# Kernel optimization log

Measured on AMD Instinct MI355X. Metric: run time of the kernel, lower is better.

The kernel has to match this reference:

```python
import jax, jax.numpy as jnp
import numpy as np

N, E, F_IN, E_IN, HID, H, C, L, OUT = 20000, 320000, 128, 64, 64, 4, 64, 4, 32


def setup_inputs() -> dict:
    key = jax.random.key(0)
    ks = jax.random.split(key, 24)
    s = 0.05
    return {
        'x': jax.random.normal(ks[0], (N, F_IN), jnp.float32),
        'edge_index': jax.random.randint(ks[1], (2, E), 0, N, jnp.int32),
        'edge_attr': jax.random.normal(ks[2], (E, E_IN), jnp.float32),
        'node_W': jax.random.normal(ks[3], (F_IN, HID), jnp.float32) * s,
        'node_b': jnp.zeros((HID,), jnp.float32),
        'eenc_W': jax.random.normal(ks[4], (E_IN, HID), jnp.float32) * s,
        'eenc_b': jnp.zeros((HID,), jnp.float32),
        'Wq': jax.random.normal(ks[5], (L, HID, H * C), jnp.float32) * s,
        'bq': jnp.zeros((L, H * C), jnp.float32),
        'Wk': jax.random.normal(ks[6], (L, HID, H * C), jnp.float32) * s,
        'bk': jnp.zeros((L, H * C), jnp.float32),
        'Wv': jax.random.normal(ks[7], (L, HID, H * C), jnp.float32) * s,
        'bv': jnp.zeros((L, H * C), jnp.float32),
        'We': jax.random.normal(ks[8], (L, HID, H * C), jnp.float32) * s,  # lin_edge, bias=False in PyG
        'Wskip': jax.random.normal(ks[9], (L, HID, HID), jnp.float32) * s,
        'bskip': jnp.zeros((L, HID), jnp.float32),
        'ln_g': jnp.ones((L, HID), jnp.float32),
        'ln_b': jnp.zeros((L, HID), jnp.float32),
        'lin_W': jax.random.normal(ks[10], (HID, OUT), jnp.float32) * s,
        'lin_b': jnp.zeros((OUT,), jnp.float32),
    }


def _layernorm(h, g, b):
    mu = h.mean(-1, keepdims=True)
    var = ((h - mu) ** 2).mean(-1, keepdims=True)
    return (h - mu) * jax.lax.rsqrt(var + 1e-5) * g + b


def _transformer_conv(h, ea, src, dst, Wq, bq, Wk, bk, Wv, bv, We, Wskip, bskip):
    n = h.shape[0]
    q = (h @ Wq + bq).reshape(n, H, C)[dst]          # [E,H,C] dst (x_i)
    k = (h @ Wk + bk).reshape(n, H, C)[src]          # [E,H,C] src (x_j)
    v = (h @ Wv + bv).reshape(n, H, C)[src]
    e = (ea @ We).reshape(-1, H, C)                  # per-edge features
    k = k + e
    alpha = (q * k).sum(-1) * (1.0 / jnp.sqrt(jnp.float32(C)))   # [E,H]
    amax = jax.ops.segment_max(alpha, dst, num_segments=n)       # segment softmax over dst
    ex = jnp.exp(alpha - amax[dst])
    denom = jax.ops.segment_sum(ex, dst, num_segments=n)
    a = ex / (denom[dst] + 1e-16)
    msg = (v + e) * a[..., None]                     # [E,H,C]
    out = jax.ops.segment_sum(msg, dst, num_segments=n)          # [N,H,C]
    out = out.mean(axis=1)                           # concat=False -> head mean
    return out + (h @ Wskip + bskip)                 # root_weight skip


def reference(x, edge_index, edge_attr, node_W, node_b, eenc_W, eenc_b,
              Wq, bq, Wk, bk, Wv, bv, We, Wskip, bskip, ln_g, ln_b, lin_W, lin_b):
    src, dst = edge_index[0], edge_index[1]
    h = x @ node_W + node_b
    ea = edge_attr @ eenc_W + eenc_b
    # layer 0: conv only (per the forward body)
    h = _transformer_conv(h, ea, src, dst, Wq[0], bq[0], Wk[0], bk[0], Wv[0], bv[0],
                          We[0], Wskip[0], bskip[0])
    # layers 1..L-1: res+ block (norm -> relu -> [dropout=id at eval] -> conv -> +res)
    for l in range(1, L):
        res = h
        z = _layernorm(h, ln_g[l], ln_b[l])
        z = jax.nn.relu(z)
        z = _transformer_conv(z, ea, src, dst, Wq[l], bq[l], Wk[l], bk[l], Wv[l], bv[l],
                              We[l], Wskip[l], bskip[l])
        h = z + res
    h = _layernorm(h, ln_g[0], ln_b[0])
    h = jax.nn.relu(h)
    return h @ lin_W + lin_b
```

## Files before the change

kernel.cpp:

```cpp
#include <hip/hip_runtime.h>
#include <hip/hip_fp16.h>
#include <math.h>

#define N_NODES 20000
#define N_EDGES 320000
#define F_IN    128
#define E_IN    64
#define HID     64
#define NH      4
#define CH      64
#define HC      256
#define L_LAYERS 4
#define OUT_DIM 32
#define WCOLS   1088

typedef _Float16 half8 __attribute__((ext_vector_type(8)));
typedef float f32x4 __attribute__((ext_vector_type(4)));

__global__ __launch_bounds__(256) void hist_dst(const int* __restrict__ dst,
                                                int* __restrict__ hist) {
    int e = blockIdx.x * 256 + threadIdx.x;
    if (e < N_EDGES) atomicAdd(&hist[dst[e]], 1);
}

__global__ __launch_bounds__(1024) void build_order(const int* __restrict__ hist,
                                                    int* __restrict__ node_order,
                                                    int* __restrict__ rank_of,
                                                    int* __restrict__ deg_rank,
                                                    int* __restrict__ new_rp,
                                                    int* __restrict__ cursor2) {
    __shared__ int bins[256];
    __shared__ int curb[256];
    __shared__ int sums[1024];
    int t = threadIdx.x;
    if (t < 256) bins[t] = 0;
    __syncthreads();
    for (int n = t; n < N_NODES; n += 1024) {
        int d = hist[n]; if (d > 255) d = 255;
        atomicAdd(&bins[d], 1);
    }
    __syncthreads();
    if (t < 256) {
        int acc = 0;
        for (int b = t + 1; b < 256; b++) acc += bins[b];
        curb[t] = acc;
    }
    __syncthreads();
    for (int n = t; n < N_NODES; n += 1024) {
        int d = hist[n];
        int b = d > 255 ? 255 : d;
        int r = atomicAdd(&curb[b], 1);
        node_order[r] = n;
        rank_of[n] = r;
        deg_rank[r] = d;
    }
    __syncthreads();
    const int CHUNK = 20;
    int base = t * CHUNK;
    int local[CHUNK];
    int s = 0;
    for (int i = 0; i < CHUNK; i++) {
        int idx = base + i;
        int vv = (idx < N_NODES) ? deg_rank[idx] : 0;
        local[i] = s;
        s += vv;
    }
    sums[t] = s;
    __syncthreads();
    for (int off = 1; off < 1024; off <<= 1) {
        int v = (t >= off) ? sums[t - off] : 0;
        __syncthreads();
        sums[t] += v;
        __syncthreads();
    }
    int excl = (t == 0) ? 0 : sums[t - 1];
    for (int i = 0; i < CHUNK; i++) {
        int idx = base + i;
        if (idx < N_NODES) {
            int p = excl + local[i];
            new_rp[idx] = p;
            cursor2[idx] = p;
        }
    }
    if (t == 1023) new_rp[N_NODES] = sums[1023];
}

__global__ __launch_bounds__(256) void compute_pos(const int* __restrict__ src,
                                                   const int* __restrict__ dst,
                                                   const int* __restrict__ rank_of,
                                                   int* __restrict__ cursor2,
                                                   int* __restrict__ eid_of,
                                                   int* __restrict__ srcrank_perm) {
    int e = blockIdx.x * 256 + threadIdx.x;
    if (e >= N_EDGES) return;
    int r = rank_of[dst[e]];
    int pos = atomicAdd(&cursor2[r], 1);
    eid_of[pos] = e;
    srcrank_perm[pos] = rank_of[src[e]];
}

__global__ __launch_bounds__(256) void permute_attr(const int* __restrict__ eid_of,
                                                    const float* __restrict__ eattr,
                                                    __half* __restrict__ attr_p) {
    int t = threadIdx.x;
    int wave = t >> 6, lane = t & 63;
    int p = blockIdx.x * 16 + wave * 4 + (lane >> 4);
    if (p >= N_EDGES) return;
    int e = eid_of[p];
    int qi = (lane & 15) * 4;
    float4 a = *(const float4*)(eattr + (size_t)e * E_IN + qi);
    __half2 h0 = __floats2half2_rn(a.x, a.y);
    __half2 h1 = __floats2half2_rn(a.z, a.w);
    uint2 packed;
    packed.x = *(unsigned int*)&h0;
    packed.y = *(unsigned int*)&h1;
    *(uint2*)(attr_p + (size_t)p * E_IN + qi) = packed;
}

__global__ __launch_bounds__(256) void make_wqeA(const float* __restrict__ Wq,
                                                 const float* __restrict__ bq,
                                                 const float* __restrict__ We,
                                                 const float* __restrict__ eW,
                                                 const float* __restrict__ eb,
                                                 float* __restrict__ Wqe2,
                                                 float* __restrict__ bqe2,
                                                 float* __restrict__ wqb,
                                                 float* __restrict__ bqb) {
    int l = blockIdx.x / HID, i = blockIdx.x % HID;
    int t = threadIdx.x;
    int h = t >> 6, j = t & 63;
    __shared__ float wrow[256];
    __shared__ float brow[256];
    const float* WqL = Wq + (size_t)l * HID * HC;
    const float* WeL = We + (size_t)l * HID * HC;
    float acc = 0.f;
    for (int c = 0; c < CH; c++)
        acc += WqL[i * HC + h * CH + c] * WeL[j * HC + h * CH + c];
    wrow[t] = acc;
    if (i == 0) {
        const float* bqL = bq + l * HC;
        float ab = 0.f;
        for (int c = 0; c < CH; c++)
            ab += bqL[h * CH + c] * WeL[j * HC + h * CH + c];
        brow[t] = ab;
    }
    __syncthreads();
    int h2 = t >> 6, m = t & 63;
    float a2 = 0.f;
    for (int jj = 0; jj < HID; jj++) a2 += wrow[h2 * 64 + jj] * eW[m * HID + jj];
    Wqe2[(size_t)l * HID * HC + i * HC + t] = a2;
    if (m == 0) {
        float aw = 0.f;
        for (int jj = 0; jj < HID; jj++) aw += wrow[h2 * 64 + jj] * eb[jj];
        wqb[l * HID * NH + i * NH + h2] = aw;
    }
    if (i == 0) {
        float ab2 = 0.f;
        for (int jj = 0; jj < HID; jj++) ab2 += brow[h2 * 64 + jj] * eW[m * HID + jj];
        bqe2[l * HC + t] = ab2;
        if (m == 0) {
            float bb = 0.f;
            for (int jj = 0; jj < HID; jj++) bb += brow[h2 * 64 + jj] * eb[jj];
            bqb[l * NH + h2] = bb;
        }
    }
}

__global__ __launch_bounds__(256) void make_weE16(const float* __restrict__ eW,
                                                  const float* __restrict__ eb,
                                                  const float* __restrict__ We,
                                                  _Float16* __restrict__ WeE16T,
                                                  float* __restrict__ beE) {
    int l = blockIdx.x / E_IN, m = blockIdx.x % E_IN;
    int t = threadIdx.x;
    const float* WeL = We + (size_t)l * HID * HC;
    float acc = 0.f;
    for (int j = 0; j < HID; j++) acc += eW[m * HID + j] * WeL[j * HC + t];
    WeE16T[((size_t)l * HC + t) * 64 + m] = (_Float16)acc;
    if (m == 0) {
        float a = 0.f;
        for (int j = 0; j < HID; j++) a += eb[j] * WeL[j * HC + t];
        beE[l * HC + t] = a;
    }
}

__global__ __launch_bounds__(256) void make_w16(
        const float* __restrict__ Wq, const float* __restrict__ Wk,
        const float* __restrict__ Wv, const float* __restrict__ Wqe2,
        const float* __restrict__ Wsk,
        const float* __restrict__ bq, const float* __restrict__ bk,
        const float* __restrict__ bv, const float* __restrict__ bqe2,
        const float* __restrict__ bsk,
        _Float16* __restrict__ W16T, float* __restrict__ biasc) {
    int l = blockIdx.x / 272;
    int cg = blockIdx.x % 272;
    int col = cg * 4 + (threadIdx.x >> 6);
    int i = threadIdx.x & 63;
    float w, b;
    if (col < 512) {
        int c = (col >> 3) * 4 + (col & 3);
        if ((col >> 2) & 1) { w = Wqe2[(size_t)l*HID*HC + i*HC + c]; b = bqe2[l*HC + c]; }
        else                { w = Wq[(size_t)l*HID*HC + i*HC + c];   b = bq[l*HC + c]; }
    } else if (col < 1024) {
        int cc = col - 512;
        int c = (cc >> 3) * 4 + (cc & 3);
        if ((cc >> 2) & 1) { w = Wv[(size_t)l*HID*HC + i*HC + c]; b = bv[l*HC + c]; }
        else               { w = Wk[(size_t)l*HID*HC + i*HC + c]; b = bk[l*HC + c]; }
    } else {
        int c = col - 1024;
        w = Wsk[(size_t)l*HID*HID + i*HID + c];  b = bsk[l*HID + c];
    }
    W16T[((size_t)l * WCOLS + col) * 64 + i] = (_Float16)w;
    if (i == 0) biasc[l * WCOLS + col] = b;
}

__global__ __launch_bounds__(256) void make_w0(const float* __restrict__ nW,
                                               const float* __restrict__ nb,
                                               _Float16* __restrict__ W0T,
                                               float* __restrict__ b0) {
    int col = blockIdx.x * 2 + (threadIdx.x >> 7);
    int i = threadIdx.x & 127;
    W0T[col * F_IN + i] = (_Float16)nW[i * HID + col];
    if (i == 0) b0[col] = nb[col];
}

__global__ __launch_bounds__(256) void node_pre0(const float* __restrict__ x,
        const int* __restrict__ node_order,
        const _Float16* __restrict__ W0T, const float* __restrict__ b0,
        const _Float16* __restrict__ W16T, const float* __restrict__ biasc,
        const float* __restrict__ wqb, const float* __restrict__ bqb,
        _Float16* __restrict__ qqw, _Float16* __restrict__ kv,
        float* __restrict__ skip, float* __restrict__ qb) {
    int t = threadIdx.x;
    int wave = t >> 6, lane = t & 63;
    int quad = lane >> 4, mrow = lane & 15;
    int base = blockIdx.x * 32;
    __shared__ _Float16 xs[32][136];
    __shared__ _Float16 zs[32][72];
    __shared__ int nord[32];
    if (t < 32) nord[t] = node_order[base + t];
    __syncthreads();
    for (int it = 0; it < 4; it++) {
        int idx = it * 256 + t;
        int m = idx >> 5, c4 = idx & 31;
        float4 a = *(const float4*)(x + (size_t)nord[m] * F_IN + c4 * 4);
        _Float16* d = &xs[m][c4 * 4];
        d[0] = (_Float16)a.x; d[1] = (_Float16)a.y;
        d[2] = (_Float16)a.z; d[3] = (_Float16)a.w;
    }
    __syncthreads();
    {
        int col = wave * 16 + mrow;
        const _Float16* w0row = W0T + (size_t)col * F_IN;
        f32x4 acc0 = {0.f, 0.f, 0.f, 0.f};
        f32x4 acc1 = {0.f, 0.f, 0.f, 0.f};
#pragma unroll
        for (int kk = 0; kk < 4; kk++) {
            half8 bfrag = *(const half8*)(w0row + kk * 32 + quad * 8);
            half8 af0 = *(const half8*)&xs[mrow][kk * 32 + quad * 8];
            half8 af1 = *(const half8*)&xs[16 + mrow][kk * 32 + quad * 8];
            acc0 = __builtin_amdgcn_mfma_f32_16x16x32_f16(af0, bfrag, acc0, 0, 0, 0);
            acc1 = __builtin_amdgcn_mfma_f32_16x16x32_f16(af1, bfrag, acc1, 0, 0, 0);
        }
        float bb = b0[col];
#pragma unroll
        for (int reg = 0; reg < 4; reg++) {
            zs[quad * 4 + reg][col] = (_Float16)(acc0[reg] + bb);
            zs[16 + quad * 4 + reg][col] = (_Float16)(acc1[reg] + bb);
        }
    }
    __syncthreads();
    if (t < 128) {
        int m = t >> 2, h4 = t & 3;
        float a = bqb[h4];
        for (int i = 0; i < HID; i++) a += (float)zs[m][i] * wqb[i * NH + h4];
        qb[(base + m) * NH + h4] = a;
    }
    half8 a00 = *(const half8*)&zs[mrow][quad * 8];
    half8 a01 = *(const half8*)&zs[mrow][32 + quad * 8];
    half8 a10 = *(const half8*)&zs[16 + mrow][quad * 8];
    half8 a11 = *(const half8*)&zs[16 + mrow][32 + quad * 8];
    int colwave = wave * 272;
    for (int tile = 0; tile < 17; tile++) {
        int colb = colwave + tile * 16;
        int col = colb + mrow;
        const _Float16* wrow = W16T + (size_t)col * 64;
        half8 b0f = *(const half8*)(wrow + quad * 8);
        half8 b1f = *(const half8*)(wrow + 32 + quad * 8);
        f32x4 acc0 = {0.f, 0.f, 0.f, 0.f};
        f32x4 acc1 = {0.f, 0.f, 0.f, 0.f};
        acc0 = __builtin_amdgcn_mfma_f32_16x16x32_f16(a00, b0f, acc0, 0, 0, 0);
        acc0 = __builtin_amdgcn_mfma_f32_16x16x32_f16(a01, b1f, acc0, 0, 0, 0);
        acc1 = __builtin_amdgcn_mfma_f32_16x16x32_f16(a10, b0f, acc1, 0, 0, 0);
        acc1 = __builtin_amdgcn_mfma_f32_16x16x32_f16(a11, b1f, acc1, 0, 0, 0);
        float bi = biasc[col];
        int seg = colb >> 9;
        int r0 = base + quad * 4;
#pragma unroll
        for (int reg = 0; reg < 4; reg++) {
            float v0 = acc0[reg] + bi;
            float v1 = acc1[reg] + bi;
            int ra = r0 + reg, rb = ra + 16;
            if (colb >= 1024) {
                int c = col - 1024;
                skip[ra * HID + c] = v0;
                skip[rb * HID + c] = v1;
            } else if (seg == 0) {
                qqw[(size_t)ra * 512 + col] = (_Float16)v0;
                qqw[(size_t)rb * 512 + col] = (_Float16)v1;
            } else {
                int c = col - 512;
                kv[(size_t)ra * 512 + c] = (_Float16)v0;
                kv[(size_t)rb * 512 + c] = (_Float16)v1;
            }
        }
    }
}

__global__ __launch_bounds__(256) void gather_edges(
        const int* __restrict__ new_rp,
        const int* __restrict__ srcrank_perm, const __half* __restrict__ attr_p,
        const __half* __restrict__ kv,
        const float* __restrict__ qb,
        const __half* qqw,
        float* numv, __half* __restrict__ numea16,
        float* __restrict__ den) {
    int wave = threadIdx.x >> 6;
    int lane = threadIdx.x & 63;
    int r = blockIdx.x * 4 + wave;
    if (r >= N_NODES) return;
    int e0 = new_rp[r], e1 = new_rp[r + 1];
    int qi = (lane & 15) * 4;
    int head = lane >> 4;
    uint4 qr = *(const uint4*)(qqw + (size_t)r * 512 + lane * 8);
    float2 q01 = __half22float2(*(__half2*)&qr.x);
    float2 q23 = __half22float2(*(__half2*)&qr.y);
    float2 w01 = __half22float2(*(__half2*)&qr.z);
    float2 w23 = __half22float2(*(__half2*)&qr.w);
    float qbh = qb[r * NH + head];
    float4 nv = make_float4(0.f, 0.f, 0.f, 0.f);
    float4 ne = make_float4(0.f, 0.f, 0.f, 0.f);
    float dsum = 0.f;
#pragma unroll 2
    for (int e = e0; e < e1; e++) {
        int s_ = srcrank_perm[e];
        uint2 araw = *(const uint2*)(attr_p + (size_t)e * E_IN + qi);
        uint4 kraw = *(const uint4*)(kv + (size_t)s_ * (2 * HC) + lane * 8);
        float2 a01 = __half22float2(*(__half2*)&araw.x);
        float2 a23 = __half22float2(*(__half2*)&araw.y);
        float2 k01 = __half22float2(*(__half2*)&kraw.x);
        float2 k23 = __half22float2(*(__half2*)&kraw.y);
        float2 v01 = __half22float2(*(__half2*)&kraw.z);
        float2 v23 = __half22float2(*(__half2*)&kraw.w);
        float rr = q01.x * k01.x + q01.y * k01.y + q23.x * k23.x + q23.y * k23.y
                 + w01.x * a01.x + w01.y * a01.y + w23.x * a23.x + w23.y * a23.y;
        rr += __shfl_xor(rr, 1);
        rr += __shfl_xor(rr, 2);
        rr += __shfl_xor(rr, 4);
        rr += __shfl_xor(rr, 8);
        float ex = __expf((rr + qbh) * 0.125f);
        nv.x += ex * v01.x; nv.y += ex * v01.y; nv.z += ex * v23.x; nv.w += ex * v23.y;
        ne.x += ex * a01.x; ne.y += ex * a01.y; ne.z += ex * a23.x; ne.w += ex * a23.y;
        dsum += ex;
    }
    *(float4*)(numv + (size_t)r * HC + lane * 4) = nv;
    __half2 n01 = __floats2half2_rn(ne.x, ne.y);
    __half2 n23 = __floats2half2_rn(ne.z, ne.w);
    uint2 np;
    np.x = *(unsigned int*)&n01;
    np.y = *(unsigned int*)&n23;
    *(uint2*)(numea16 + (size_t)r * HC + lane * 4) = np;
    if ((lane & 15) == 0) den[r * NH + head] = dsum;
}

__global__ __launch_bounds__(256) void node_mid(
        const int* __restrict__ node_order,
        const float* numv,
        const __half* __restrict__ numea16,
        const float* __restrict__ den_g,
        float* skip,
        float* __restrict__ h,
        const _Float16* __restrict__ WeE16T,
        const float* __restrict__ beE,
        int add_res,
        const _Float16* __restrict__ W16T,
        const float* __restrict__ biasc,
        const float* __restrict__ wqb, const float* __restrict__ bqb,
        const float* __restrict__ g, const float* __restrict__ be,
        _Float16* qqw, _Float16* __restrict__ kv,
        float* __restrict__ qb) {
    int t = threadIdx.x;
    int wave = t >> 6, lane = t & 63;
    int quad = lane >> 4, mrow = lane & 15;
    int base = blockIdx.x * 16;
    __shared__ _Float16 ea16[16][264];
    __shared__ float hsum[4][16][64];
    __shared__ float hnew[16][64];
    __shared__ _Float16 zs[16][72];
    __shared__ float bsh[256];
    __shared__ float dsh[64];
    __shared__ int nord[16];
    if (t < 16) nord[t] = node_order[base + t];
    if (t < 64) dsh[t] = den_g[base * 4 + t];
    bsh[t] = beE[t];
    for (int it = 0; it < 2; it++) {
        int idx = it * 256 + t;
        int m = idx >> 5, c8 = idx & 31;
        uint4 raw = *(const uint4*)(numea16 + (size_t)(base + m) * HC + c8 * 8);
        *(uint4*)&ea16[m][c8 * 8] = raw;
    }
    __syncthreads();
    {
        int hd = wave;
        half8 a_lo = *(const half8*)&ea16[mrow][hd * 64 + quad * 8];
        half8 a_hi = *(const half8*)&ea16[mrow][hd * 64 + 32 + quad * 8];
        for (int nt = 0; nt < 4; nt++) {
            int c = nt * 16 + mrow;
            const _Float16* bp = WeE16T + (size_t)(hd * 64 + c) * 64;
            half8 b_lo = *(const half8*)(bp + quad * 8);
            half8 b_hi = *(const half8*)(bp + 32 + quad * 8);
            f32x4 acc = {0.f, 0.f, 0.f, 0.f};
            acc = __builtin_amdgcn_mfma_f32_16x16x32_f16(a_lo, b_lo, acc, 0, 0, 0);
            acc = __builtin_amdgcn_mfma_f32_16x16x32_f16(a_hi, b_hi, acc, 0, 0, 0);
            int tp = hd * 64 + c;
#pragma unroll
            for (int reg = 0; reg < 4; reg++) {
                int m = quad * 4 + reg;
                float nvv = numv[(size_t)(base + m) * HC + tp];
                float dd = dsh[m * 4 + hd];
                hsum[hd][m][c] = (nvv + acc[reg] + dd * bsh[tp]) / (dd + 1e-16f) * 0.25f;
            }
        }
    }
    __syncthreads();
    for (int it = 0; it < 4; it++) {
        int idx = it * 256 + t;
        int m = idx >> 6, c = idx & 63;
        float s = hsum[0][m][c] + hsum[1][m][c] + hsum[2][m][c] + hsum[3][m][c]
                + skip[(base + m) * HID + c];
        if (add_res) s += h[nord[m] * HID + c];
        h[nord[m] * HID + c] = s;
        hnew[m][c] = s;
    }
    __syncthreads();
    for (int it = 0; it < 4; it++) {
        int m = it * 4 + wave;
        float val = hnew[m][lane];
        float mu = val;
        for (int o = 32; o > 0; o >>= 1) mu += __shfl_xor(mu, o);
        mu *= (1.f / 64.f);
        float d = val - mu;
        float var = d * d;
        for (int o = 32; o > 0; o >>= 1) var += __shfl_xor(var, o);
        var *= (1.f / 64.f);
        val = fmaxf(d * rsqrtf(var + 1e-5f) * g[lane] + be[lane], 0.f);
        zs[m][lane] = (_Float16)val;
    }
    __syncthreads();
    if (t < 64) {
        int m = t >> 2, h4 = t & 3;
        float a = bqb[h4];
        for (int i = 0; i < HID; i++) a += (float)zs[m][i] * wqb[i * NH + h4];
        qb[(base + m) * NH + h4] = a;
    }
    half8 a00 = *(const half8*)&zs[mrow][quad * 8];
    half8 a01 = *(const half8*)&zs[mrow][32 + quad * 8];
    int colwave = wave * 272;
    for (int tile = 0; tile < 17; tile++) {
        int colb = colwave + tile * 16;
        int col = colb + mrow;
        const _Float16* wrow = W16T + (size_t)col * 64;
        half8 b0f = *(const half8*)(wrow + quad * 8);
        half8 b1f = *(const half8*)(wrow + 32 + quad * 8);
        f32x4 acc = {0.f, 0.f, 0.f, 0.f};
        acc = __builtin_amdgcn_mfma_f32_16x16x32_f16(a00, b0f, acc, 0, 0, 0);
        acc = __builtin_amdgcn_mfma_f32_16x16x32_f16(a01, b1f, acc, 0, 0, 0);
        float bi = biasc[col];
        int seg = colb >> 9;
#pragma unroll
        for (int reg = 0; reg < 4; reg++) {
            float v0 = acc[reg] + bi;
            int ra = base + quad * 4 + reg;
            if (colb >= 1024) {
                skip[ra * HID + (col - 1024)] = v0;
            } else if (seg == 0) {
                qqw[(size_t)ra * 512 + col] = (_Float16)v0;
            } else {
                kv[(size_t)ra * 512 + (col - 512)] = (_Float16)v0;
            }
        }
    }
}

__global__ __launch_bounds__(256) void node_fin(
        const int* __restrict__ node_order,
        const float* __restrict__ numv,
        const __half* __restrict__ numea16,
        const float* __restrict__ den_g,
        const float* __restrict__ skip,
        const float* __restrict__ h,
        const _Float16* __restrict__ WeE16T, const float* __restrict__ beE,
        const float* __restrict__ g, const float* __restrict__ be,
        const float* __restrict__ linW, const float* __restrict__ linb,
        float* __restrict__ out) {
    int t = threadIdx.x;
    int wave = t >> 6, lane = t & 63;
    int quad = lane >> 4, mrow = lane & 15;
    int base = blockIdx.x * 16;
    __shared__ _Float16 ea16[16][264];
    __shared__ float hsum[4][16][64];
    __shared__ float hnew[16][64];
    __shared__ float bsh[256];
    __shared__ float dsh[64];
    __shared__ int nord[16];
    if (t < 16) nord[t] = node_order[base + t];
    if (t < 64) dsh[t] = den_g[base * 4 + t];
    bsh[t] = beE[t];
    for (int it = 0; it < 2; it++) {
        int idx = it * 256 + t;
        int m = idx >> 5, c8 = idx & 31;
        uint4 raw = *(const uint4*)(numea16 + (size_t)(base + m) * HC + c8 * 8);
        *(uint4*)&ea16[m][c8 * 8] = raw;
    }
    __syncthreads();
    {
        int hd = wave;
        half8 a_lo = *(const half8*)&ea16[mrow][hd * 64 + quad * 8];
        half8 a_hi = *(const half8*)&ea16[mrow][hd * 64 + 32 + quad * 8];
        for (int nt = 0; nt < 4; nt++) {
            int c = nt * 16 + mrow;
            const _Float16* bp = WeE16T + (size_t)(hd * 64 + c) * 64;
            half8 b_lo = *(const half8*)(bp + quad * 8);
            half8 b_hi = *(const half8*)(bp + 32 + quad * 8);
            f32x4 acc = {0.f, 0.f, 0.f, 0.f};
            acc = __builtin_amdgcn_mfma_f32_16x16x32_f16(a_lo, b_lo, acc, 0, 0, 0);
            acc = __builtin_amdgcn_mfma_f32_16x16x32_f16(a_hi, b_hi, acc, 0, 0, 0);
            int tp = hd * 64 + c;
#pragma unroll
            for (int reg = 0; reg < 4; reg++) {
                int m = quad * 4 + reg;
                float nvv = numv[(size_t)(base + m) * HC + tp];
                float dd = dsh[m * 4 + hd];
                hsum[hd][m][c] = (nvv + acc[reg] + dd * bsh[tp]) / (dd + 1e-16f) * 0.25f;
            }
        }
    }
    __syncthreads();
    for (int it = 0; it < 4; it++) {
        int idx = it * 256 + t;
        int m = idx >> 6, c = idx & 63;
        float s = hsum[0][m][c] + hsum[1][m][c] + hsum[2][m][c] + hsum[3][m][c]
                + skip[(base + m) * HID + c] + h[nord[m] * HID + c];
        hnew[m][c] = s;
    }
    __syncthreads();
    for (int it = 0; it < 4; it++) {
        int m = it * 4 + wave;
        float val = hnew[m][lane];
        float mu = val;
        for (int o = 32; o > 0; o >>= 1) mu += __shfl_xor(mu, o);
        mu *= (1.f / 64.f);
        float d = val - mu;
        float var = d * d;
        for (int o = 32; o > 0; o >>= 1) var += __shfl_xor(var, o);
        var *= (1.f / 64.f);
        hnew[m][lane] = fmaxf(d * rsqrtf(var + 1e-5f) * g[lane] + be[lane], 0.f);
    }
    __syncthreads();
    for (int it = 0; it < 2; it++) {
        int idx = it * 256 + t;
        int m = idx >> 5, col = idx & 31;
        float a = linb[col];
        for (int i = 0; i < HID; i++) a += hnew[m][i] * linW[i * OUT_DIM + col];
        out[nord[m] * OUT_DIM + col] = a;
    }
}

extern "C" void kernel_launch(void* const* d_in, const int* in_sizes, int n_in,
                              void* d_out, int out_size, void* d_ws, size_t ws_size,
                              hipStream_t stream) {
    const float* x      = (const float*)d_in[0];
    const int*   ei     = (const int*)d_in[1];
    const float* eattr  = (const float*)d_in[2];
    const float* node_W = (const float*)d_in[3];
    const float* node_b = (const float*)d_in[4];
    const float* eenc_W = (const float*)d_in[5];
    const float* eenc_b = (const float*)d_in[6];
    const float* Wq     = (const float*)d_in[7];
    const float* bq     = (const float*)d_in[8];
    const float* Wk     = (const float*)d_in[9];
    const float* bk     = (const float*)d_in[10];
    const float* Wv     = (const float*)d_in[11];
    const float* bv     = (const float*)d_in[12];
    const float* We     = (const float*)d_in[13];
    const float* Wskip  = (const float*)d_in[14];
    const float* bskip  = (const float*)d_in[15];
    const float* ln_g   = (const float*)d_in[16];
    const float* ln_b   = (const float*)d_in[17];
    const float* lin_W  = (const float*)d_in[18];
    const float* lin_b  = (const float*)d_in[19];
    float* out = (float*)d_out;

    const int* src = ei;
    const int* dst = ei + N_EDGES;

    float* ws = (float*)d_ws;
    __half* attr_p = (__half*)ws; ws += (size_t)N_EDGES * E_IN / 2;
    float* h    = ws; ws += N_NODES * HID;
    _Float16* qqw = (_Float16*)ws; ws += (size_t)N_NODES * HC;
    float* numv = (float*)qqw;
    __half* numea16 = (__half*)ws; ws += (size_t)N_NODES * HC / 2;
    _Float16* kv = (_Float16*)ws; ws += (size_t)N_NODES * HC;
    float* skip = ws; ws += N_NODES * HID;
    float* den  = ws; ws += N_NODES * NH;
    float* qb   = ws; ws += N_NODES * NH;
    float* Wqe2 = ws; ws += (size_t)L_LAYERS * HID * HC;
    float* bqe2 = ws; ws += L_LAYERS * HC;
    float* wqb  = ws; ws += L_LAYERS * HID * NH;
    float* bqb  = ws; ws += L_LAYERS * NH;
    _Float16* WeE16T = (_Float16*)ws; ws += (size_t)L_LAYERS * HC * HID / 2;
    float* beE  = ws; ws += L_LAYERS * HC;
    _Float16* W16T = (_Float16*)ws; ws += (size_t)L_LAYERS * WCOLS * HID / 2;
    float* biasc = ws; ws += L_LAYERS * WCOLS;
    _Float16* W0T = (_Float16*)ws; ws += HID * F_IN / 2;
    float* b0  = ws; ws += HID;
    int* ip = (int*)ws;
    int* hist         = ip; ip += N_NODES;
    int* node_order   = ip; ip += N_NODES;
    int* rank_of      = ip; ip += N_NODES;
    int* deg_rank     = ip; ip += N_NODES;
    int* new_rp       = ip; ip += N_NODES + 4;
    int* cursor2      = ip; ip += N_NODES;
    int* srcrank_perm = ip; ip += N_EDGES;
    int* eid_of       = ip; ip += N_EDGES;

    hipMemsetAsync(hist, 0, N_NODES * sizeof(int), stream);
    hist_dst<<<(N_EDGES + 255) / 256, 256, 0, stream>>>(dst, hist);
    build_order<<<1, 1024, 0, stream>>>(hist, node_order, rank_of, deg_rank,
                                        new_rp, cursor2);

    make_wqeA<<<L_LAYERS * HID, 256, 0, stream>>>(Wq, bq, We, eenc_W, eenc_b,
                                                  Wqe2, bqe2, wqb, bqb);
    make_weE16<<<L_LAYERS * E_IN, 256, 0, stream>>>(eenc_W, eenc_b, We, WeE16T, beE);
    make_w16<<<L_LAYERS * 272, 256, 0, stream>>>(Wq, Wk, Wv, Wqe2, Wskip,
                                                 bq, bk, bv, bqe2, bskip,
                                                 W16T, biasc);
    make_w0<<<HID / 2, 256, 0, stream>>>(node_W, node_b, W0T, b0);

    compute_pos<<<(N_EDGES + 255) / 256, 256, 0, stream>>>(src, dst, rank_of, cursor2,
                                                           eid_of, srcrank_perm);
    permute_attr<<<N_EDGES / 16, 256, 0, stream>>>(eid_of, eattr, attr_p);

    node_pre0<<<N_NODES / 32, 256, 0, stream>>>(
        x, node_order, W0T, b0, W16T, biasc, wqb, bqb, qqw, kv, skip, qb);

    for (int l = 0; l < L_LAYERS; l++) {
        gather_edges<<<(N_NODES + 3) / 4, 256, 0, stream>>>(
            new_rp, srcrank_perm, attr_p, (const __half*)kv, qb,
            (const __half*)qqw, numv, numea16, den);
        if (l < L_LAYERS - 1) {
            node_mid<<<N_NODES / 16, 256, 0, stream>>>(
                node_order, numv, numea16, den, skip, h,
                WeE16T + (size_t)l * HC * HID, beE + l * HC,
                (l > 0) ? 1 : 0,
                W16T + (size_t)(l + 1) * WCOLS * HID, biasc + (l + 1) * WCOLS,
                wqb + (l + 1) * HID * NH, bqb + (l + 1) * NH,
                ln_g + (l + 1) * HID, ln_b + (l + 1) * HID,
                qqw, kv, qb);
        } else {
            node_fin<<<N_NODES / 16, 256, 0, stream>>>(
                node_order, numv, numea16, den, skip, h,
                WeE16T + (size_t)l * HC * HID, beE + l * HC,
                ln_g, ln_b, lin_W, lin_b, out);
        }
    }
}
```

Baseline: 733.6 us.

## Fold head-mean into edge-weight GEMM and vectorize node projection stores

The per-head edge-feature GEMM plus the 4-way hsum reduction is replaced by one K=256 MFMA against a concatenated weight matrix. The 1/den scaling is applied to the edge aggregates before the GEMM, so the head mean falls out of the matrix product. The projection GEMMs swap MFMA operand order so each lane holds four consecutive columns, which allows half4/float4 stores instead of scalar scattered stores. The q-bias reduction is split across more threads with shuffles, and h is kept in rank order, which drops the node_order indirection in node_mid. In exchange, aggregates are rescaled in fp16 before the matmul, which may shift precision slightly.

```diff
diff --git a/kernel.cpp b/kernel.cpp
--- a/kernel.cpp
+++ b/kernel.cpp
@@ -15,6 +15,7 @@
 #define WCOLS   1088
 
 typedef _Float16 half8 __attribute__((ext_vector_type(8)));
+typedef _Float16 half4 __attribute__((ext_vector_type(4)));
 typedef float f32x4 __attribute__((ext_vector_type(4)));
 
 __global__ __launch_bounds__(256) void hist_dst(const int* __restrict__ dst,
@@ -166,21 +167,27 @@
     }
 }
 
-__global__ __launch_bounds__(256) void make_weE16(const float* __restrict__ eW,
-                                                  const float* __restrict__ eb,
-                                                  const float* __restrict__ We,
-                                                  _Float16* __restrict__ WeE16T,
-                                                  float* __restrict__ beE) {
-    int l = blockIdx.x / E_IN, m = blockIdx.x % E_IN;
+__global__ __launch_bounds__(256) void make_wcat(const float* __restrict__ eW,
+                                                 const float* __restrict__ eb,
+                                                 const float* __restrict__ We,
+                                                 _Float16* __restrict__ Wcat16,
+                                                 float* __restrict__ beE) {
+    int l = blockIdx.x / 64, c = blockIdx.x % 64;
     int t = threadIdx.x;
-    const float* WeL = We + (size_t)l * HID * HC;
+    __shared__ float sh[4][64];
+    {
+        int j = t & 63, h = t >> 6;
+        sh[h][j] = We[(size_t)l * HID * HC + j * HC + h * 64 + c];
+    }
+    __syncthreads();
+    int h = t >> 6, m = t & 63;
     float acc = 0.f;
-    for (int j = 0; j < HID; j++) acc += eW[m * HID + j] * WeL[j * HC + t];
-    WeE16T[((size_t)l * HC + t) * 64 + m] = (_Float16)acc;
-    if (m == 0) {
+    for (int j = 0; j < HID; j++) acc += eW[m * HID + j] * sh[h][j];
+    Wcat16[((size_t)l * 64 + c) * 256 + t] = (_Float16)acc;
+    if (t < 4) {
         float a = 0.f;
-        for (int j = 0; j < HID; j++) a += eb[j] * WeL[j * HC + t];
-        beE[l * HC + t] = a;
+        for (int j = 0; j < HID; j++) a += eb[j] * sh[t][j];
+        beE[l * HC + t * 64 + c] = a;
     }
 }
 
@@ -250,31 +257,35 @@
     }
     __syncthreads();
     {
-        int col = wave * 16 + mrow;
-        const _Float16* w0row = W0T + (size_t)col * F_IN;
+        int colb = wave * 16;
+        const _Float16* w0row = W0T + (size_t)(colb + mrow) * F_IN;
         f32x4 acc0 = {0.f, 0.f, 0.f, 0.f};
         f32x4 acc1 = {0.f, 0.f, 0.f, 0.f};
 #pragma unroll
         for (int kk = 0; kk < 4; kk++) {
-            half8 bfrag = *(const half8*)(w0row + kk * 32 + quad * 8);
-            half8 af0 = *(const half8*)&xs[mrow][kk * 32 + quad * 8];
-            half8 af1 = *(const half8*)&xs[16 + mrow][kk * 32 + quad * 8];
-            acc0 = __builtin_amdgcn_mfma_f32_16x16x32_f16(af0, bfrag, acc0, 0, 0, 0);
-            acc1 = __builtin_amdgcn_mfma_f32_16x16x32_f16(af1, bfrag, acc1, 0, 0, 0);
-        }
-        float bb = b0[col];
-#pragma unroll
-        for (int reg = 0; reg < 4; reg++) {
-            zs[quad * 4 + reg][col] = (_Float16)(acc0[reg] + bb);
-            zs[16 + quad * 4 + reg][col] = (_Float16)(acc1[reg] + bb);
-        }
-    }
-    __syncthreads();
-    if (t < 128) {
-        int m = t >> 2, h4 = t & 3;
-        float a = bqb[h4];
-        for (int i = 0; i < HID; i++) a += (float)zs[m][i] * wqb[i * NH + h4];
-        qb[(base + m) * NH + h4] = a;
+            half8 wfrag = *(const half8*)(w0row + kk * 32 + quad * 8);
+            half8 xf0 = *(const half8*)&xs[mrow][kk * 32 + quad * 8];
+            half8 xf1 = *(const half8*)&xs[16 + mrow][kk * 32 + quad * 8];
+            acc0 = __builtin_amdgcn_mfma_f32_16x16x32_f16(wfrag, xf0, acc0, 0, 0, 0);
+            acc1 = __builtin_amdgcn_mfma_f32_16x16x32_f16(wfrag, xf1, acc1, 0, 0, 0);
+        }
+        float4 bb = *(const float4*)(b0 + colb + quad * 4);
+        half4 h0v = {(_Float16)(acc0[0] + bb.x), (_Float16)(acc0[1] + bb.y),
+                     (_Float16)(acc0[2] + bb.z), (_Float16)(acc0[3] + bb.w)};
+        half4 h1v = {(_Float16)(acc1[0] + bb.x), (_Float16)(acc1[1] + bb.y),
+                     (_Float16)(acc1[2] + bb.z), (_Float16)(acc1[3] + bb.w)};
+        *(half4*)&zs[mrow][colb + quad * 4] = h0v;
+        *(half4*)&zs[16 + mrow][colb + quad * 4] = h1v;
+    }
+    __syncthreads();
+    {
+        int p = t >> 1, s4 = t & 1;
+        int m = p >> 2, h4 = p & 3;
+        float a = 0.f;
+        for (int i = s4 * 32; i < s4 * 32 + 32; i++)
+            a += (float)zs[m][i] * wqb[i * NH + h4];
+        a += __shfl_xor(a, 1);
+        if (s4 == 0) qb[(base + m) * NH + h4] = a + bqb[h4];
     }
     half8 a00 = *(const half8*)&zs[mrow][quad * 8];
     half8 a01 = *(const half8*)&zs[mrow][32 + quad * 8];
@@ -283,35 +294,34 @@
     int colwave = wave * 272;
     for (int tile = 0; tile < 17; tile++) {
         int colb = colwave + tile * 16;
-        int col = colb + mrow;
-        const _Float16* wrow = W16T + (size_t)col * 64;
+        const _Float16* wrow = W16T + (size_t)(colb + mrow) * 64;
         half8 b0f = *(const half8*)(wrow + quad * 8);
         half8 b1f = *(const half8*)(wrow + 32 + quad * 8);
         f32x4 acc0 = {0.f, 0.f, 0.f, 0.f};
         f32x4 acc1 = {0.f, 0.f, 0.f, 0.f};
-        acc0 = __builtin_amdgcn_mfma_f32_16x16x32_f16(a00, b0f, acc0, 0, 0, 0);
-        acc0 = __builtin_amdgcn_mfma_f32_16x16x32_f16(a01, b1f, acc0, 0, 0, 0);
-        acc1 = __builtin_amdgcn_mfma_f32_16x16x32_f16(a10, b0f, acc1, 0, 0, 0);
-        acc1 = __builtin_amdgcn_mfma_f32_16x16x32_f16(a11, b1f, acc1, 0, 0, 0);
-        float bi = biasc[col];
-        int seg = colb >> 9;
-        int r0 = base + quad * 4;
-#pragma unroll
-        for (int reg = 0; reg < 4; reg++) {
-            float v0 = acc0[reg] + bi;
-            float v1 = acc1[reg] + bi;
-            int ra = r0 + reg, rb = ra + 16;
-            if (colb >= 1024) {
-                int c = col - 1024;
-                skip[ra * HID + c] = v0;
-                skip[rb * HID + c] = v1;
-            } else if (seg == 0) {
-                qqw[(size_t)ra * 512 + col] = (_Float16)v0;
-                qqw[(size_t)rb * 512 + col] = (_Float16)v1;
+        acc0 = __builtin_amdgcn_mfma_f32_16x16x32_f16(b0f, a00, acc0, 0, 0, 0);
+        acc0 = __builtin_amdgcn_mfma_f32_16x16x32_f16(b1f, a01, acc0, 0, 0, 0);
+        acc1 = __builtin_amdgcn_mfma_f32_16x16x32_f16(b0f, a10, acc1, 0, 0, 0);
+        acc1 = __builtin_amdgcn_mfma_f32_16x16x32_f16(b1f, a11, acc1, 0, 0, 0);
+        float4 bi4 = *(const float4*)(biasc + colb + quad * 4);
+        int wc = colb + quad * 4;
+        int ra = base + mrow, rb = ra + 16;
+        float v00 = acc0[0] + bi4.x, v01 = acc0[1] + bi4.y;
+        float v02 = acc0[2] + bi4.z, v03 = acc0[3] + bi4.w;
+        float v10 = acc1[0] + bi4.x, v11 = acc1[1] + bi4.y;
+        float v12 = acc1[2] + bi4.z, v13 = acc1[3] + bi4.w;
+        if (colb >= 1024) {
+            *(float4*)(skip + ra * HID + (wc - 1024)) = make_float4(v00, v01, v02, v03);
+            *(float4*)(skip + rb * HID + (wc - 1024)) = make_float4(v10, v11, v12, v13);
+        } else {
+            half4 p0 = {(_Float16)v00, (_Float16)v01, (_Float16)v02, (_Float16)v03};
+            half4 p1 = {(_Float16)v10, (_Float16)v11, (_Float16)v12, (_Float16)v13};
+            if (colb < 512) {
+                *(half4*)(qqw + (size_t)ra * 512 + wc) = p0;
+                *(half4*)(qqw + (size_t)rb * 512 + wc) = p1;
             } else {
-                int c = col - 512;
-                kv[(size_t)ra * 512 + c] = (_Float16)v0;
-                kv[(size_t)rb * 512 + c] = (_Float16)v1;
+                *(half4*)(kv + (size_t)ra * 512 + (wc - 512)) = p0;
+                *(half4*)(kv + (size_t)rb * 512 + (wc - 512)) = p1;
             }
         }
     }
@@ -374,13 +384,12 @@
 }
 
 __global__ __launch_bounds__(256) void node_mid(
-        const int* __restrict__ node_order,
         const float* numv,
         const __half* __restrict__ numea16,
         const float* __restrict__ den_g,
         float* skip,
-        float* __restrict__ h,
-        const _Float16* __restrict__ WeE16T,
+        float* __restrict__ hg,
+        const _Float16* __restrict__ Wcat16,
         const float* __restrict__ beE,
         int add_res,
         const _Float16* __restrict__ W16T,
@@ -394,52 +403,59 @@
     int quad = lane >> 4, mrow = lane & 15;
     int base = blockIdx.x * 16;
     __shared__ _Float16 ea16[16][264];
-    __shared__ float hsum[4][16][64];
     __shared__ float hnew[16][64];
     __shared__ _Float16 zs[16][72];
     __shared__ float bsh[256];
-    __shared__ float dsh[64];
-    __shared__ int nord[16];
-    if (t < 16) nord[t] = node_order[base + t];
-    if (t < 64) dsh[t] = den_g[base * 4 + t];
+    __shared__ float rr_[64];
+    __shared__ float ff_[64];
+    if (t < 64) {
+        float dd = den_g[base * 4 + t];
+        float rc = 1.f / (dd + 1e-16f);
+        rr_[t] = rc;
+        ff_[t] = dd * rc;
+    }
     bsh[t] = beE[t];
+    __syncthreads();
     for (int it = 0; it < 2; it++) {
         int idx = it * 256 + t;
         int m = idx >> 5, c8 = idx & 31;
+        float rc = rr_[m * 4 + (c8 >> 3)];
         uint4 raw = *(const uint4*)(numea16 + (size_t)(base + m) * HC + c8 * 8);
+        __half2* hp = (__half2*)&raw;
+#pragma unroll
+        for (int i = 0; i < 4; i++) {
+            float2 f = __half22float2(hp[i]);
+            hp[i] = __floats2half2_rn(f.x * rc, f.y * rc);
+        }
         *(uint4*)&ea16[m][c8 * 8] = raw;
     }
     __syncthreads();
     {
-        int hd = wave;
-        half8 a_lo = *(const half8*)&ea16[mrow][hd * 64 + quad * 8];
-        half8 a_hi = *(const half8*)&ea16[mrow][hd * 64 + 32 + quad * 8];
-        for (int nt = 0; nt < 4; nt++) {
-            int c = nt * 16 + mrow;
-            const _Float16* bp = WeE16T + (size_t)(hd * 64 + c) * 64;
-            half8 b_lo = *(const half8*)(bp + quad * 8);
-            half8 b_hi = *(const half8*)(bp + 32 + quad * 8);
-            f32x4 acc = {0.f, 0.f, 0.f, 0.f};
-            acc = __builtin_amdgcn_mfma_f32_16x16x32_f16(a_lo, b_lo, acc, 0, 0, 0);
-            acc = __builtin_amdgcn_mfma_f32_16x16x32_f16(a_hi, b_hi, acc, 0, 0, 0);
-            int tp = hd * 64 + c;
-#pragma unroll
-            for (int reg = 0; reg < 4; reg++) {
-                int m = quad * 4 + reg;
-                float nvv = numv[(size_t)(base + m) * HC + tp];
-                float dd = dsh[m * 4 + hd];
-                hsum[hd][m][c] = (nvv + acc[reg] + dd * bsh[tp]) / (dd + 1e-16f) * 0.25f;
-            }
-        }
+        int cb = wave * 16;
+        f32x4 acc = {0.f, 0.f, 0.f, 0.f};
+#pragma unroll
+        for (int kk = 0; kk < 8; kk++) {
+            half8 af = *(const half8*)&ea16[mrow][kk * 32 + quad * 8];
+            half8 bf = *(const half8*)(Wcat16 + (size_t)(cb + mrow) * 256 + kk * 32 + quad * 8);
+            acc = __builtin_amdgcn_mfma_f32_16x16x32_f16(af, bf, acc, 0, 0, 0);
+        }
+#pragma unroll
+        for (int reg = 0; reg < 4; reg++)
+            hnew[quad * 4 + reg][cb + mrow] = acc[reg];
     }
     __syncthreads();
     for (int it = 0; it < 4; it++) {
         int idx = it * 256 + t;
         int m = idx >> 6, c = idx & 63;
-        float s = hsum[0][m][c] + hsum[1][m][c] + hsum[2][m][c] + hsum[3][m][c]
-                + skip[(base + m) * HID + c];
-        if (add_res) s += h[nord[m] * HID + c];
-        h[nord[m] * HID + c] = s;
+        float s = hnew[m][c];
+#pragma unroll
+        for (int hh = 0; hh < 4; hh++)
+            s += numv[(size_t)(base + m) * HC + hh * 64 + c] * rr_[m * 4 + hh]
+               + ff_[m * 4 + hh] * bsh[hh * 64 + c];
+        s *= 0.25f;
+        s += skip[(base + m) * HID + c];
+        if (add_res) s += hg[(base + m) * HID + c];
+        hg[(base + m) * HID + c] = s;
         hnew[m][c] = s;
     }
     __syncthreads();
@@ -457,37 +473,38 @@
         zs[m][lane] = (_Float16)val;
     }
     __syncthreads();
-    if (t < 64) {
-        int m = t >> 2, h4 = t & 3;
-        float a = bqb[h4];
-        for (int i = 0; i < HID; i++) a += (float)zs[m][i] * wqb[i * NH + h4];
-        qb[(base + m) * NH + h4] = a;
+    {
+        int p = t >> 2, s4 = t & 3;
+        int m = p >> 2, h4 = p & 3;
+        float a = 0.f;
+        for (int i = s4 * 16; i < s4 * 16 + 16; i++)
+            a += (float)zs[m][i] * wqb[i * NH + h4];
+        a += __shfl_xor(a, 1);
+        a += __shfl_xor(a, 2);
+        if (s4 == 0) qb[(base + m) * NH + h4] = a + bqb[h4];
     }
     half8 a00 = *(const half8*)&zs[mrow][quad * 8];
     half8 a01 = *(const half8*)&zs[mrow][32 + quad * 8];
     int colwave = wave * 272;
     for (int tile = 0; tile < 17; tile++) {
         int colb = colwave + tile * 16;
-        int col = colb + mrow;
-        const _Float16* wrow = W16T + (size_t)col * 64;
+        const _Float16* wrow = W16T + (size_t)(colb + mrow) * 64;
         half8 b0f = *(const half8*)(wrow + quad * 8);
         half8 b1f = *(const half8*)(wrow + 32 + quad * 8);
         f32x4 acc = {0.f, 0.f, 0.f, 0.f};
-        acc = __builtin_amdgcn_mfma_f32_16x16x32_f16(a00, b0f, acc, 0, 0, 0);
-        acc = __builtin_amdgcn_mfma_f32_16x16x32_f16(a01, b1f, acc, 0, 0, 0);
-        float bi = biasc[col];
-        int seg = colb >> 9;
-#pragma unroll
-        for (int reg = 0; reg < 4; reg++) {
-            float v0 = acc[reg] + bi;
-            int ra = base + quad * 4 + reg;
-            if (colb >= 1024) {
-                skip[ra * HID + (col - 1024)] = v0;
-            } else if (seg == 0) {
-                qqw[(size_t)ra * 512 + col] = (_Float16)v0;
-            } else {
-                kv[(size_t)ra * 512 + (col - 512)] = (_Float16)v0;
-            }
+        acc = __builtin_amdgcn_mfma_f32_16x16x32_f16(b0f, a00, acc, 0, 0, 0);
+        acc = __builtin_amdgcn_mfma_f32_16x16x32_f16(b1f, a01, acc, 0, 0, 0);
+        float4 bi4 = *(const float4*)(biasc + colb + quad * 4);
+        int wc = colb + quad * 4;
+        int ra = base + mrow;
+        float v0 = acc[0] + bi4.x, v1 = acc[1] + bi4.y;
+        float v2 = acc[2] + bi4.z, v3 = acc[3] + bi4.w;
+        if (colb >= 1024) {
+            *(float4*)(skip + ra * HID + (wc - 1024)) = make_float4(v0, v1, v2, v3);
+        } else {
+            half4 pk = {(_Float16)v0, (_Float16)v1, (_Float16)v2, (_Float16)v3};
+            if (colb < 512) *(half4*)(qqw + (size_t)ra * 512 + wc) = pk;
+            else            *(half4*)(kv + (size_t)ra * 512 + (wc - 512)) = pk;
         }
     }
 }
@@ -498,8 +515,8 @@
         const __half* __restrict__ numea16,
         const float* __restrict__ den_g,
         const float* __restrict__ skip,
-        const float* __restrict__ h,
-        const _Float16* __restrict__ WeE16T, const float* __restrict__ beE,
+        const float* __restrict__ hg,
+        const _Float16* __restrict__ Wcat16, const float* __restrict__ beE,
         const float* __restrict__ g, const float* __restrict__ be,
         const float* __restrict__ linW, const float* __restrict__ linb,
         float* __restrict__ out) {
@@ -508,49 +525,58 @@
     int quad = lane >> 4, mrow = lane & 15;
     int base = blockIdx.x * 16;
     __shared__ _Float16 ea16[16][264];
-    __shared__ float hsum[4][16][64];
     __shared__ float hnew[16][64];
     __shared__ float bsh[256];
-    __shared__ float dsh[64];
+    __shared__ float rr_[64];
+    __shared__ float ff_[64];
     __shared__ int nord[16];
     if (t < 16) nord[t] = node_order[base + t];
-    if (t < 64) dsh[t] = den_g[base * 4 + t];
+    if (t < 64) {
+        float dd = den_g[base * 4 + t];
+        float rc = 1.f / (dd + 1e-16f);
+        rr_[t] = rc;
+        ff_[t] = dd * rc;
+    }
     bsh[t] = beE[t];
+    __syncthreads();
     for (int it = 0; it < 2; it++) {
         int idx = it * 256 + t;
         int m = idx >> 5, c8 = idx & 31;
+        float rc = rr_[m * 4 + (c8 >> 3)];
         uint4 raw = *(const uint4*)(numea16 + (size_t)(base + m) * HC + c8 * 8);
+        __half2* hp = (__half2*)&raw;
+#pragma unroll
+        for (int i = 0; i < 4; i++) {
+            float2 f = __half22float2(hp[i]);
+            hp[i] = __floats2half2_rn(f.x * rc, f.y * rc);
+        }
         *(uint4*)&ea16[m][c8 * 8] = raw;
     }
     __syncthreads();
     {
-        int hd = wave;
-        half8 a_lo = *(const half8*)&ea16[mrow][hd * 64 + quad * 8];
-        half8 a_hi = *(const half8*)&ea16[mrow][hd * 64 + 32 + quad * 8];
-        for (int nt = 0; nt < 4; nt++) {
-            int c = nt * 16 + mrow;
-            const _Float16* bp = WeE16T + (size_t)(hd * 64 + c) * 64;
-            half8 b_lo = *(const half8*)(bp + quad * 8);
-            half8 b_hi = *(const half8*)(bp + 32 + quad * 8);
-            f32x4 acc = {0.f, 0.f, 0.f, 0.f};
-            acc = __builtin_amdgcn_mfma_f32_16x16x32_f16(a_lo, b_lo, acc, 0, 0, 0);
-            acc = __builtin_amdgcn_mfma_f32_16x16x32_f16(a_hi, b_hi, acc, 0, 0, 0);
-            int tp = hd * 64 + c;
-#pragma unroll
-            for (int reg = 0; reg < 4; reg++) {
-                int m = quad * 4 + reg;
-                float nvv = numv[(size_t)(base + m) * HC + tp];
-                float dd = dsh[m * 4 + hd];
-                hsum[hd][m][c] = (nvv + acc[reg] + dd * bsh[tp]) / (dd + 1e-16f) * 0.25f;
-            }
-        }
+        int cb = wave * 16;
+        f32x4 acc = {0.f, 0.f, 0.f, 0.f};
+#pragma unroll
+        for (int kk = 0; kk < 8; kk++) {
+            half8 af = *(const half8*)&ea16[mrow][kk * 32 + quad * 8];
+            half8 bf = *(const half8*)(Wcat16 + (size_t)(cb + mrow) * 256 + kk * 32 + quad * 8);
+            acc = __builtin_amdgcn_mfma_f32_16x16x32_f16(af, bf, acc, 0, 0, 0);
+        }
+#pragma unroll
+        for (int reg = 0; reg < 4; reg++)
+            hnew[quad * 4 + reg][cb + mrow] = acc[reg];
     }
     __syncthreads();
     for (int it = 0; it < 4; it++) {
         int idx = it * 256 + t;
         int m = idx >> 6, c = idx & 63;
-        float s = hsum[0][m][c] + hsum[1][m][c] + hsum[2][m][c] + hsum[3][m][c]
-                + skip[(base + m) * HID + c] + h[nord[m] * HID + c];
+        float s = hnew[m][c];
+#pragma unroll
+        for (int hh = 0; hh < 4; hh++)
+            s += numv[(size_t)(base + m) * HC + hh * 64 + c] * rr_[m * 4 + hh]
+               + ff_[m * 4 + hh] * bsh[hh * 64 + c];
+        s *= 0.25f;
+        s += skip[(base + m) * HID + c] + hg[(base + m) * HID + c];
         hnew[m][c] = s;
     }
     __syncthreads();
@@ -618,7 +644,7 @@
     float* bqe2 = ws; ws += L_LAYERS * HC;
     float* wqb  = ws; ws += L_LAYERS * HID * NH;
     float* bqb  = ws; ws += L_LAYERS * NH;
-    _Float16* WeE16T = (_Float16*)ws; ws += (size_t)L_LAYERS * HC * HID / 2;
+    _Float16* Wcat16 = (_Float16*)ws; ws += (size_t)L_LAYERS * 64 * 256 / 2;
     float* beE  = ws; ws += L_LAYERS * HC;
     _Float16* W16T = (_Float16*)ws; ws += (size_t)L_LAYERS * WCOLS * HID / 2;
     float* biasc = ws; ws += L_LAYERS * WCOLS;
@@ -641,7 +667,7 @@
 
     make_wqeA<<<L_LAYERS * HID, 256, 0, stream>>>(Wq, bq, We, eenc_W, eenc_b,
                                                   Wqe2, bqe2, wqb, bqb);
-    make_weE16<<<L_LAYERS * E_IN, 256, 0, stream>>>(eenc_W, eenc_b, We, WeE16T, beE);
+    make_wcat<<<L_LAYERS * 64, 256, 0, stream>>>(eenc_W, eenc_b, We, Wcat16, beE);
     make_w16<<<L_LAYERS * 272, 256, 0, stream>>>(Wq, Wk, Wv, Wqe2, Wskip,
                                                  bq, bk, bv, bqe2, bskip,
                                                  W16T, biasc);
@@ -660,8 +686,8 @@
             (const __half*)qqw, numv, numea16, den);
         if (l < L_LAYERS - 1) {
             node_mid<<<N_NODES / 16, 256, 0, stream>>>(
-                node_order, numv, numea16, den, skip, h,
-                WeE16T + (size_t)l * HC * HID, beE + l * HC,
+                numv, numea16, den, skip, h,
+                Wcat16 + (size_t)l * 64 * 256, beE + l * HC,
                 (l > 0) ? 1 : 0,
                 W16T + (size_t)(l + 1) * WCOLS * HID, biasc + (l + 1) * WCOLS,
                 wqb + (l + 1) * HID * NH, bqb + (l + 1) * NH,
@@ -670,7 +696,7 @@
         } else {
             node_fin<<<N_NODES / 16, 256, 0, stream>>>(
                 node_order, numv, numea16, den, skip, h,
-                WeE16T + (size_t)l * HC * HID, beE + l * HC,
+                Wcat16 + (size_t)l * 64 * 256, beE + l * HC,
                 ln_g, ln_b, lin_W, lin_b, out);
         }
     }
```

Result: faster. 674.4 us (-8.1%).
